# Optimization experiments

Measured on AMD Instinct MI355X. Metric: run time of the kernel, lower is better.

The kernel has to match this reference:

```python
import jax, jax.numpy as jnp
import numpy as np

STRIDES = (8, 16, 32, 64, 128)
TOPK = 1000          # fixed candidate count (jit-friendly stand-in for boolean masking)
SCORE_TH = 0.05      # from `score > 0.05` in postProcessing
IOU_TH = 0.5         # standard FCOS NMS threshold


def _decode_level(cls, cnt, reg, stride):
    # cls [B,C,H,W], cnt [B,1,H,W], reg [B,4,H,W]
    B, C, H, W = cls.shape
    p_cls = jax.nn.sigmoid(cls).transpose(0, 2, 3, 1).reshape(B, H * W, C)
    p_cnt = jax.nn.sigmoid(cnt).transpose(0, 2, 3, 1).reshape(B, H * W, 1)
    p_reg = jnp.exp(reg).transpose(0, 2, 3, 1).reshape(B, H * W, 4)  # (l,t,r,b) distances
    ys = (jnp.arange(H, dtype=cls.dtype) + 0.5) * stride
    xs = (jnp.arange(W, dtype=cls.dtype) + 0.5) * stride
    yy, xx = jnp.meshgrid(ys, xs, indexing='ij')
    cx = xx.reshape(-1)[None, :]  # [1,HW]
    cy = yy.reshape(-1)[None, :]
    boxes = jnp.stack([cx - p_reg[..., 0], cy - p_reg[..., 1],
                       cx + p_reg[..., 2], cy + p_reg[..., 3]], axis=-1)  # [B,HW,4]
    return p_cls, p_cnt, boxes


def _iou_matrix(b):
    # b [K,4] (x1,y1,x2,y2) -> [K,K]
    area = jnp.clip(b[:, 2] - b[:, 0], 0) * jnp.clip(b[:, 3] - b[:, 1], 0)
    x1 = jnp.maximum(b[:, None, 0], b[None, :, 0])
    y1 = jnp.maximum(b[:, None, 1], b[None, :, 1])
    x2 = jnp.minimum(b[:, None, 2], b[None, :, 2])
    y2 = jnp.minimum(b[:, None, 3], b[None, :, 3])
    inter = jnp.clip(x2 - x1, 0) * jnp.clip(y2 - y1, 0)
    return inter / (area[:, None] + area[None, :] - inter + 1e-9)


def _nms_keep(boxes, scores):
    # boxes [K,4] sorted by descending score, scores [K] -> keep mask [K]
    K = boxes.shape[0]
    iou = _iou_matrix(boxes)
    idx = jnp.arange(K)
    keep0 = scores > SCORE_TH
    def body(i, keep):
        sup = (iou[i] > IOU_TH) & (idx > i) & keep[i]
        return keep & ~sup
    return jax.lax.fori_loop(0, K, body, keep0)


def _detect(levels):
    cls_l, cnt_l, box_l = [], [], []
    for (c, n, r), s in zip(levels, STRIDES):
        pc, pn, pb = _decode_level(c, n, r, s)
        cls_l.append(pc); cnt_l.append(pn); box_l.append(pb)
    cls = jnp.concatenate(cls_l, 1)    # [B,N,C]
    boxes = jnp.concatenate(box_l, 1)  # [B,N,4]
    score = cls.max(-1)                # per original: score from cls (cnt unused in score)
    kind = cls.argmax(-1)
    top_s, top_i = jax.lax.top_k(score, TOPK)                      # [B,K]
    top_b = jnp.take_along_axis(boxes, top_i[..., None], axis=1)   # [B,K,4]
    top_k = jnp.take_along_axis(kind, top_i, axis=1)               # [B,K]
    keep = jax.vmap(_nms_keep)(top_b, top_s)                       # [B,K] bool
    out = jnp.concatenate([top_b,
                           top_k[..., None].astype(cls.dtype),
                           top_s[..., None],
                           keep[..., None].astype(cls.dtype)], axis=-1)  # [B,K,7]
    return out


def setup_inputs() -> dict:
    key = jax.random.key(0)
    B, C = 16, 20
    hw = [(128, 160), (64, 80), (32, 40), (16, 20), (8, 10)]
    names = []
    for p in (3, 4, 5, 6, 7):
        names += [f'cls_p{p}', f'cnt_p{p}', f'reg_p{p}']
    ks = jax.random.split(key, len(names))
    inp = {}
    for li, (H, W) in enumerate(hw):
        inp[f'cls_p{li+3}'] = jax.random.normal(ks[3*li+0], (B, C, H, W), jnp.float32)
        inp[f'cnt_p{li+3}'] = jax.random.normal(ks[3*li+1], (B, 1, H, W), jnp.float32)
        inp[f'reg_p{li+3}'] = jax.random.normal(ks[3*li+2], (B, 4, H, W), jnp.float32)
    return inp


def reference(cls_p3, cnt_p3, reg_p3, cls_p4, cnt_p4, reg_p4,
              cls_p5, cnt_p5, reg_p5, cls_p6, cnt_p6, reg_p6,
              cls_p7, cnt_p7, reg_p7):
    levels = [(cls_p3, cnt_p3, reg_p3), (cls_p4, cnt_p4, reg_p4),
              (cls_p5, cnt_p5, reg_p5), (cls_p6, cnt_p6, reg_p6),
              (cls_p7, cnt_p7, reg_p7)]
    return _detect(levels)
```

## Files before the change

### kernel.cpp

```cpp
#include <hip/hip_runtime.h>
#include <math.h>

#define BATCH 16
#define NCH 20
#define NPOS 27280
#define NTOP 1000
#define KW 16
#define NBIN 4096
#define CANDCAP 4096
#define NSLICE 7

typedef unsigned long long u64;
typedef unsigned int u32;

__device__ __align__(16) u32 g_sb[BATCH * NPOS];
__device__ unsigned char g_kind[BATCH * NPOS];
__device__ u32 g_hph[BATCH * NSLICE * NBIN];
__device__ u32 g_suf[BATCH * NBIN];
__device__ u32 g_cnt[BATCH * NBIN];
__device__ u32 g_dcnt[BATCH * NBIN];
__device__ int g_thr[BATCH];
__device__ int g_ncand[BATCH];
__device__ u64 g_cand[BATCH * CANDCAP];
__device__ float4 g_box[BATCH * NTOP];
__device__ float g_score[BATCH * NTOP];
__device__ u64 g_mask[BATCH * NTOP * KW];
__device__ unsigned char g_rowsup[BATCH * NTOP];

__device__ __forceinline__ int digit_of(u32 sb) {
  int d = ((int)sb - 0x3F000000) >> 11;
  return d < 0 ? 0 : (d > (NBIN - 1) ? (NBIN - 1) : d);
}

__device__ __forceinline__ int jj(int j) { return j + (j >> 6); }
#define SKEWCAP (NTOP + NTOP / 64 + 1)

__global__ __launch_bounds__(1024) void k1_score(
    const float* __restrict__ c3, const float* __restrict__ c4,
    const float* __restrict__ c5, const float* __restrict__ c6,
    const float* __restrict__ c7) {
  int b = blockIdx.y, bx = blockIdx.x, tid = threadIdx.x;
  __shared__ u32 lh[NBIN];
  for (int j = tid; j < NBIN; j += 1024) lh[j] = 0;
  __syncthreads();

  int n0 = bx * 4096 + tid * 4;
  if (n0 < NPOS) {
    const float* cls; int off, hw;
    if (n0 < 20480)      { cls = c3; off = 0;     hw = 20480; }
    else if (n0 < 25600) { cls = c4; off = 20480; hw = 5120;  }
    else if (n0 < 26880) { cls = c5; off = 25600; hw = 1280;  }
    else if (n0 < 27200) { cls = c6; off = 26880; hw = 320;   }
    else                 { cls = c7; off = 27200; hw = 80;    }
    int local = n0 - off;
    const float4* p = (const float4*)(cls + (size_t)b * NCH * hw + local);
    int s4 = hw >> 2;
    float4 best = p[0];
    int k0 = 0, k1 = 0, k2 = 0, k3 = 0;
    for (int c = 1; c < NCH; ++c) {
      float4 v = p[(size_t)c * s4];
      if (v.x > best.x) { best.x = v.x; k0 = c; }
      if (v.y > best.y) { best.y = v.y; k1 = c; }
      if (v.z > best.z) { best.z = v.z; k2 = c; }
      if (v.w > best.w) { best.w = v.w; k3 = c; }
    }
    float bb[4] = {best.x, best.y, best.z, best.w};
    u32 sb[4];
#pragma unroll
    for (int i = 0; i < 4; ++i) {
      float e = (float)exp(-(double)bb[i]);
      float s = 1.0f / (1.0f + e);
      sb[i] = __float_as_uint(s);
      atomicAdd(&lh[digit_of(sb[i])], 1u);
    }
    uint4 sb4; sb4.x = sb[0]; sb4.y = sb[1]; sb4.z = sb[2]; sb4.w = sb[3];
    *(uint4*)&g_sb[(size_t)b * NPOS + n0] = sb4;
    u32 kind4 = (u32)k0 | ((u32)k1 << 8) | ((u32)k2 << 16) | ((u32)k3 << 24);
    *(u32*)&g_kind[(size_t)b * NPOS + n0] = kind4;
  }
  __syncthreads();
  u32* ph = g_hph + ((size_t)b * NSLICE + bx) * NBIN;
  for (int j = tid; j < NBIN; j += 1024) ph[j] = lh[j];
}

__global__ __launch_bounds__(1024) void k2_scan() {
  int b = blockIdx.x, tid = threadIdx.x;
  int lane = tid & 63, wid = tid >> 6;
  __shared__ u32 wsum[16];
  u32 c[4];
#pragma unroll
  for (int k = 0; k < 4; ++k) {
    int d = 4 * tid + k;
    u32 s = 0;
    for (int p = 0; p < NSLICE; ++p) s += g_hph[((size_t)b * NSLICE + p) * NBIN + d];
    c[k] = s;
    g_cnt[b * NBIN + d] = s;
  }
  u32 tot = c[0] + c[1] + c[2] + c[3];
  u32 s = tot;
#pragma unroll
  for (int off = 1; off < 64; off <<= 1) {
    u32 v = __shfl_down(s, off);
    if (lane + off < 64) s += v;
  }
  if (lane == 0) wsum[wid] = s;
  __syncthreads();
  u32 wexcl = 0;
  for (int w2 = wid + 1; w2 < 16; ++w2) wexcl += wsum[w2];
  u32 e = wexcl + (s - tot);
  u32 e3 = e;
  u32 e2 = e3 + c[3];
  u32 e1 = e2 + c[2];
  u32 e0 = e1 + c[1];
  g_suf[b * NBIN + 4 * tid + 3] = e3;
  g_suf[b * NBIN + 4 * tid + 2] = e2;
  g_suf[b * NBIN + 4 * tid + 1] = e1;
  g_suf[b * NBIN + 4 * tid + 0] = e0;
  if (e3 < NTOP && NTOP <= e3 + c[3]) { g_thr[b] = 4 * tid + 3; g_ncand[b] = (int)(e3 + c[3]); }
  if (e2 < NTOP && NTOP <= e2 + c[2]) { g_thr[b] = 4 * tid + 2; g_ncand[b] = (int)(e2 + c[2]); }
  if (e1 < NTOP && NTOP <= e1 + c[1]) { g_thr[b] = 4 * tid + 1; g_ncand[b] = (int)(e1 + c[1]); }
  if (e0 < NTOP && NTOP <= e0 + c[0]) { g_thr[b] = 4 * tid + 0; g_ncand[b] = (int)(e0 + c[0]); }
  for (int j = tid; j < NBIN; j += 1024) g_dcnt[b * NBIN + j] = 0;
}

__global__ __launch_bounds__(1024) void k3_compact() {
  int b = blockIdx.y, bx = blockIdx.x, tid = threadIdx.x;
  int n0 = bx * 4096 + tid * 4;
  if (n0 >= NPOS) return;
  int thr = g_thr[b];
  uint4 sb4 = *(const uint4*)&g_sb[(size_t)b * NPOS + n0];
  u32 sb[4] = {sb4.x, sb4.y, sb4.z, sb4.w};
#pragma unroll
  for (int i = 0; i < 4; ++i) {
    int d = digit_of(sb[i]);
    if (d >= thr) {
      u32 slot = g_suf[b * NBIN + d] + atomicAdd(&g_dcnt[b * NBIN + d], 1u);
      if (slot < CANDCAP)
        g_cand[b * CANDCAP + slot] = ((u64)sb[i] << 15) | (u32)(NPOS - (n0 + i));
    }
  }
}

__global__ __launch_bounds__(1024) void k4_rank(
    const float* __restrict__ r3, const float* __restrict__ r4,
    const float* __restrict__ r5, const float* __restrict__ r6,
    const float* __restrict__ r7, float* __restrict__ out) {
  int b = blockIdx.x, tid = threadIdx.x;
  int ncand = g_ncand[b];
  if (ncand > CANDCAP) ncand = CANDCAP;
  for (int i = tid; i < ncand; i += 1024) {
    u64 k = g_cand[b * CANDCAP + i];
    int d = digit_of((u32)(k >> 15));
    u32 gs = g_suf[b * NBIN + d];
    u32 ge = gs + g_cnt[b * NBIN + d];
    if (ge > (u32)ncand) ge = (u32)ncand;
    int rank = (int)gs;
    for (u32 j = gs; j < ge; ++j) rank += (int)(g_cand[b * CANDCAP + j] > k);
    if (rank >= NTOP) continue;
    u32 n = (u32)NPOS - (u32)(k & 0x7FFFu);
    float sc = __uint_as_float((u32)(k >> 15));
    const float* reg; int off, hw, lvl;
    if (n < 20480)      { reg = r3; off = 0;     hw = 20480; lvl = 0; }
    else if (n < 25600) { reg = r4; off = 20480; hw = 5120;  lvl = 1; }
    else if (n < 26880) { reg = r5; off = 25600; hw = 1280;  lvl = 2; }
    else if (n < 27200) { reg = r6; off = 26880; hw = 320;   lvl = 3; }
    else                { reg = r7; off = 27200; hw = 80;    lvl = 4; }
    int local = (int)n - off;
    int W = 160 >> lvl;
    int hh = local / W, ww = local - hh * W;
    float stride = (float)(8 << lvl);
    const float* rp = reg + (size_t)b * 4 * hw + local;
    float e0 = expf(rp[0]);
    float e1 = expf(rp[(size_t)hw]);
    float e2 = expf(rp[(size_t)2 * hw]);
    float e3 = expf(rp[(size_t)3 * hw]);
    float cx = (ww + 0.5f) * stride, cy = (hh + 0.5f) * stride;
    float x1 = cx - e0, y1 = cy - e1, x2 = cx + e2, y2 = cy + e3;
    int ok = b * NTOP + rank;
    g_box[ok] = make_float4(x1, y1, x2, y2);
    g_score[ok] = sc;
    float* o = out + (size_t)ok * 7;
    o[0] = x1; o[1] = y1; o[2] = x2; o[3] = y2;
    o[4] = (float)g_kind[(size_t)b * NPOS + n];
    o[5] = sc;
  }
}

__global__ __launch_bounds__(256) void k5_mask() {
  int b = blockIdx.y;
  int ig = blockIdx.x;
  int tid = threadIdx.x;
  int lane = tid & 63;
  int jlo = ig * 16;
  int nst = NTOP - jlo;
  __shared__ float4 shbox[SKEWCAP];
  __shared__ float shA[SKEWCAP];
  const float4* boxes = g_box + b * NTOP;
  for (int j = tid; j < nst; j += 256) {
    float4 bj = boxes[jlo + j];
    shbox[jj(j)] = bj;
    shA[jj(j)] = fmaxf(bj.z - bj.x, 0.f) * fmaxf(bj.w - bj.y, 0.f);
  }
  __syncthreads();
  int i = jlo + (tid >> 4);
  int t = tid & 15;
  u64 word = 0;
  if (i < NTOP) {
    float4 bi = shbox[jj(i - jlo)];
    float aarea = shA[jj(i - jlo)];
    int j0 = t * 64;
    int jbeg = (j0 > i + 1) ? j0 : i + 1;
    int jend = (j0 + 64 < NTOP) ? j0 + 64 : NTOP;
    for (int j = jbeg; j < jend; ++j) {
      float4 bj = shbox[jj(j - jlo)];
      float barea = shA[jj(j - jlo)];
      float ix1 = fmaxf(bi.x, bj.x), iy1 = fmaxf(bi.y, bj.y);
      float ix2 = fminf(bi.z, bj.z), iy2 = fminf(bi.w, bj.w);
      float inter = fmaxf(ix2 - ix1, 0.f) * fmaxf(iy2 - iy1, 0.f);
      if (inter + inter > aarea + barea - inter + 1e-9f)
        word |= 1ull << (j - j0);
    }
    g_mask[((size_t)b * NTOP + i) * KW + t] = word;
  }
  u64 b16 = __ballot(word != 0);
  int rg = lane >> 4;
  if (t == 0 && i < NTOP)
    g_rowsup[b * NTOP + i] = (unsigned char)(((b16 >> (rg * 16)) & 0xFFFFull) ? 1 : 0);
}

__global__ __launch_bounds__(64) void k6_greedy(float* __restrict__ out) {
  int b = blockIdx.x;
  int lane = threadIdx.x;
  int col = lane & 15, g = lane >> 4;
  const u64* mask = g_mask + (size_t)b * NTOP * KW;

  u64 mdiag[KW];
  float s[KW];
  unsigned char rs[KW];
#pragma unroll
  for (int w = 0; w < KW; ++w) {
    int k = w * 64 + lane;
    mdiag[w] = (k < NTOP) ? mask[(size_t)k * KW + w] : 0ull;
    s[w] = (k < NTOP) ? g_score[b * NTOP + k] : 0.f;
    rs[w] = (k < NTOP) ? g_rowsup[b * NTOP + k] : (unsigned char)0;
  }

  u64 remv = 0;
  for (int w = 0; w < KW; ++w) {
    int k = w * 64 + lane;
    u64 keep0 = __ballot(k < NTOP && s[w] > 0.05f);
    u64 gate = __ballot(rs[w] != 0);
    u64 cur = keep0 & ~__shfl(remv, w);
    u64 rem = cur & gate;
    u64 acc = 0;
    while (rem) {
      int i = __ffsll(rem) - 1;
      u64 v = __shfl(mdiag[w], i);
      rem &= ~(v | (1ull << i));
      cur &= ~v;
      acc |= (1ull << i);
    }
    u64 upd = 0;
#pragma unroll
    for (int r = 0; r < 16; ++r) {
      int i2 = g * 16 + r;
      if ((acc >> i2) & 1ull)
        upd |= mask[(size_t)(w * 64 + i2) * KW + col];
    }
    upd |= __shfl_xor(upd, 16);
    upd |= __shfl_xor(upd, 32);
    remv |= upd;
    if (k < NTOP) out[(size_t)(b * NTOP + k) * 7 + 6] = (float)((cur >> lane) & 1ull);
  }
}

extern "C" void kernel_launch(void* const* d_in, const int* in_sizes, int n_in,
                              void* d_out, int out_size, void* d_ws, size_t ws_size,
                              hipStream_t stream) {
  const float* c3 = (const float*)d_in[0];
  const float* r3 = (const float*)d_in[2];
  const float* c4 = (const float*)d_in[3];
  const float* r4 = (const float*)d_in[5];
  const float* c5 = (const float*)d_in[6];
  const float* r5 = (const float*)d_in[8];
  const float* c6 = (const float*)d_in[9];
  const float* r6 = (const float*)d_in[11];
  const float* c7 = (const float*)d_in[12];
  const float* r7 = (const float*)d_in[14];
  float* out = (float*)d_out;

  hipLaunchKernelGGL(k1_score, dim3(NSLICE, BATCH), dim3(1024), 0, stream,
                     c3, c4, c5, c6, c7);
  hipLaunchKernelGGL(k2_scan, dim3(BATCH), dim3(1024), 0, stream);
  hipLaunchKernelGGL(k3_compact, dim3(NSLICE, BATCH), dim3(1024), 0, stream);
  hipLaunchKernelGGL(k4_rank, dim3(BATCH), dim3(1024), 0, stream,
                     r3, r4, r5, r6, r7, out);
  hipLaunchKernelGGL(k5_mask, dim3(63, BATCH), dim3(256), 0, stream);
  hipLaunchKernelGGL(k6_greedy, dim3(BATCH), dim3(64), 0, stream, out);
}
```

Before: 63.08 us.

## Spread scoring, ranking across more blocks and transpose NMS mask layout

Doubles the number of slices in the score and compact kernels, so each thread handles two positions instead of four and twice as many blocks run per batch. Splits the rank kernel over 8 smaller blocks per batch instead of one large block. Transposes the suppression mask to column-major so the greedy kernel's diagonal and update loads are coalesced across lanes. The aim is better GPU occupancy on small per-batch kernels, at the cost of twice as many partial histograms for the scan kernel to sum.

```diff
diff --git a/kernel.cpp b/kernel.cpp
--- a/kernel.cpp
+++ b/kernel.cpp
@@ -8,7 +8,8 @@
 #define KW 16
 #define NBIN 4096
 #define CANDCAP 4096
-#define NSLICE 7
+#define NSLICE 14
+#define SLICEPOS 2048
 
 typedef unsigned long long u64;
 typedef unsigned int u32;
@@ -24,7 +25,7 @@
 __device__ u64 g_cand[BATCH * CANDCAP];
 __device__ float4 g_box[BATCH * NTOP];
 __device__ float g_score[BATCH * NTOP];
-__device__ u64 g_mask[BATCH * NTOP * KW];
+__device__ u64 g_maskT[BATCH * KW * NTOP];
 __device__ unsigned char g_rowsup[BATCH * NTOP];
 
 __device__ __forceinline__ int digit_of(u32 sb) {
@@ -44,7 +45,7 @@
   for (int j = tid; j < NBIN; j += 1024) lh[j] = 0;
   __syncthreads();
 
-  int n0 = bx * 4096 + tid * 4;
+  int n0 = bx * SLICEPOS + tid * 2;
   if (n0 < NPOS) {
     const float* cls; int off, hw;
     if (n0 < 20480)      { cls = c3; off = 0;     hw = 20480; }
@@ -53,30 +54,28 @@
     else if (n0 < 27200) { cls = c6; off = 26880; hw = 320;   }
     else                 { cls = c7; off = 27200; hw = 80;    }
     int local = n0 - off;
-    const float4* p = (const float4*)(cls + (size_t)b * NCH * hw + local);
-    int s4 = hw >> 2;
-    float4 best = p[0];
-    int k0 = 0, k1 = 0, k2 = 0, k3 = 0;
+    const float2* p = (const float2*)(cls + (size_t)b * NCH * hw + local);
+    int s2 = hw >> 1;
+    float2 best = p[0];
+    int k0 = 0, k1 = 0;
     for (int c = 1; c < NCH; ++c) {
-      float4 v = p[(size_t)c * s4];
+      float2 v = p[(size_t)c * s2];
       if (v.x > best.x) { best.x = v.x; k0 = c; }
       if (v.y > best.y) { best.y = v.y; k1 = c; }
-      if (v.z > best.z) { best.z = v.z; k2 = c; }
-      if (v.w > best.w) { best.w = v.w; k3 = c; }
-    }
-    float bb[4] = {best.x, best.y, best.z, best.w};
-    u32 sb[4];
-#pragma unroll
-    for (int i = 0; i < 4; ++i) {
+    }
+    float bb[2] = {best.x, best.y};
+    u32 sb[2];
+#pragma unroll
+    for (int i = 0; i < 2; ++i) {
       float e = (float)exp(-(double)bb[i]);
       float s = 1.0f / (1.0f + e);
       sb[i] = __float_as_uint(s);
       atomicAdd(&lh[digit_of(sb[i])], 1u);
     }
-    uint4 sb4; sb4.x = sb[0]; sb4.y = sb[1]; sb4.z = sb[2]; sb4.w = sb[3];
-    *(uint4*)&g_sb[(size_t)b * NPOS + n0] = sb4;
-    u32 kind4 = (u32)k0 | ((u32)k1 << 8) | ((u32)k2 << 16) | ((u32)k3 << 24);
-    *(u32*)&g_kind[(size_t)b * NPOS + n0] = kind4;
+    uint2 sb2; sb2.x = sb[0]; sb2.y = sb[1];
+    *(uint2*)&g_sb[(size_t)b * NPOS + n0] = sb2;
+    *(unsigned short*)&g_kind[(size_t)b * NPOS + n0] =
+        (unsigned short)((u32)k0 | ((u32)k1 << 8));
   }
   __syncthreads();
   u32* ph = g_hph + ((size_t)b * NSLICE + bx) * NBIN;
@@ -125,13 +124,13 @@
 
 __global__ __launch_bounds__(1024) void k3_compact() {
   int b = blockIdx.y, bx = blockIdx.x, tid = threadIdx.x;
-  int n0 = bx * 4096 + tid * 4;
+  int n0 = bx * SLICEPOS + tid * 2;
   if (n0 >= NPOS) return;
   int thr = g_thr[b];
-  uint4 sb4 = *(const uint4*)&g_sb[(size_t)b * NPOS + n0];
-  u32 sb[4] = {sb4.x, sb4.y, sb4.z, sb4.w};
-#pragma unroll
-  for (int i = 0; i < 4; ++i) {
+  uint2 sb2 = *(const uint2*)&g_sb[(size_t)b * NPOS + n0];
+  u32 sb[2] = {sb2.x, sb2.y};
+#pragma unroll
+  for (int i = 0; i < 2; ++i) {
     int d = digit_of(sb[i]);
     if (d >= thr) {
       u32 slot = g_suf[b * NBIN + d] + atomicAdd(&g_dcnt[b * NBIN + d], 1u);
@@ -141,14 +140,14 @@
   }
 }
 
-__global__ __launch_bounds__(1024) void k4_rank(
+__global__ __launch_bounds__(256) void k4_rank(
     const float* __restrict__ r3, const float* __restrict__ r4,
     const float* __restrict__ r5, const float* __restrict__ r6,
     const float* __restrict__ r7, float* __restrict__ out) {
-  int b = blockIdx.x, tid = threadIdx.x;
+  int b = blockIdx.y, bx = blockIdx.x, tid = threadIdx.x;
   int ncand = g_ncand[b];
   if (ncand > CANDCAP) ncand = CANDCAP;
-  for (int i = tid; i < ncand; i += 1024) {
+  for (int i = bx * 256 + tid; i < ncand; i += 8 * 256) {
     u64 k = g_cand[b * CANDCAP + i];
     int d = digit_of((u32)(k >> 15));
     u32 gs = g_suf[b * NBIN + d];
@@ -220,7 +219,7 @@
       if (inter + inter > aarea + barea - inter + 1e-9f)
         word |= 1ull << (j - j0);
     }
-    g_mask[((size_t)b * NTOP + i) * KW + t] = word;
+    g_maskT[((size_t)b * KW + t) * NTOP + i] = word;
   }
   u64 b16 = __ballot(word != 0);
   int rg = lane >> 4;
@@ -232,7 +231,7 @@
   int b = blockIdx.x;
   int lane = threadIdx.x;
   int col = lane & 15, g = lane >> 4;
-  const u64* mask = g_mask + (size_t)b * NTOP * KW;
+  const u64* maskT = g_maskT + (size_t)b * KW * NTOP;
 
   u64 mdiag[KW];
   float s[KW];
@@ -240,7 +239,7 @@
 #pragma unroll
   for (int w = 0; w < KW; ++w) {
     int k = w * 64 + lane;
-    mdiag[w] = (k < NTOP) ? mask[(size_t)k * KW + w] : 0ull;
+    mdiag[w] = (k < NTOP) ? maskT[(size_t)w * NTOP + k] : 0ull;
     s[w] = (k < NTOP) ? g_score[b * NTOP + k] : 0.f;
     rs[w] = (k < NTOP) ? g_rowsup[b * NTOP + k] : (unsigned char)0;
   }
@@ -264,8 +263,10 @@
 #pragma unroll
     for (int r = 0; r < 16; ++r) {
       int i2 = g * 16 + r;
-      if ((acc >> i2) & 1ull)
-        upd |= mask[(size_t)(w * 64 + i2) * KW + col];
+      if ((acc >> i2) & 1ull) {
+        int row = w * 64 + i2;
+        if (row < NTOP) upd |= maskT[(size_t)col * NTOP + row];
+      }
     }
     upd |= __shfl_xor(upd, 16);
     upd |= __shfl_xor(upd, 32);
@@ -293,7 +294,7 @@
                      c3, c4, c5, c6, c7);
   hipLaunchKernelGGL(k2_scan, dim3(BATCH), dim3(1024), 0, stream);
   hipLaunchKernelGGL(k3_compact, dim3(NSLICE, BATCH), dim3(1024), 0, stream);
-  hipLaunchKernelGGL(k4_rank, dim3(BATCH), dim3(1024), 0, stream,
+  hipLaunchKernelGGL(k4_rank, dim3(8, BATCH), dim3(256), 0, stream,
                      r3, r4, r5, r6, r7, out);
   hipLaunchKernelGGL(k5_mask, dim3(63, BATCH), dim3(256), 0, stream);
   hipLaunchKernelGGL(k6_greedy, dim3(BATCH), dim3(64), 0, stream, out);
```

Measured after the change: 58.01 us. 8.0% less time.
